# Performance work log

Hardware: AMD Instinct MI355X
Metric: run time of the kernel (lower is better)

## Reference

```python
import jax, jax.numpy as jnp
import numpy as np

V, E, H, S, B, L = 10000, 512, 1024, 64, 64, 2

def setup_inputs() -> dict:
    key = jax.random.key(0)
    ks = iter(jax.random.split(key, 32))
    k_emb = 0.1
    k_h = float(np.sqrt(1.0 / H))
    inp = {}
    inp['inputs'] = jax.random.randint(next(ks), (S, B), 0, V)
    inp['init_hidden'] = jnp.zeros((L, B, H), jnp.float32)
    inp['emb_table'] = jax.random.uniform(next(ks), (V, E), jnp.float32, -k_emb, k_emb)
    in_feats = [E + H, 2 * H]
    for l in range(L):
        fi = in_feats[l]
        for nm in ('Wr', 'Wz', 'Wh'):
            inp[f'{nm}{l}'] = jax.random.uniform(next(ks), (fi, H), jnp.float32, -k_h, k_h)
        for nm in ('br', 'bz', 'bh'):
            inp[f'{nm}{l}'] = jax.random.uniform(next(ks), (H,), jnp.float32, -k_h, k_h)
    inp['Wfc0'] = jax.random.uniform(next(ks), (H, H), jnp.float32, -k_h, k_h)
    inp['bfc0'] = jax.random.uniform(next(ks), (H,), jnp.float32, -k_h, k_h)
    inp['Wout'] = jax.random.uniform(next(ks), (H, V), jnp.float32, -0.1, 0.1)
    inp['bout'] = jnp.zeros((V,), jnp.float32)
    return inp

def reference(inputs, init_hidden, emb_table,
              Wr0, Wz0, Wh0, br0, bz0, bh0,
              Wr1, Wz1, Wh1, br1, bz1, bh1,
              Wfc0, bfc0, Wout, bout):
    layers = [(Wr0, br0, Wz0, bz0, Wh0, bh0), (Wr1, br1, Wz1, bz1, Wh1, bh1)]
    fcs = [(Wfc0, bfc0)]
    emb = emb_table[inputs]  # [S, B, E]

    def step(h_prev, xt):
        # h_prev: [L, B, H]; xt: [B, E]
        x = xt
        hs = []
        for l, (Wr, br, Wz, bz, Wh, bh) in enumerate(layers):
            h = h_prev[l]
            cat = jnp.concatenate([x, h], axis=1)
            r = jax.nn.sigmoid(cat @ Wr + br)
            z = jax.nn.sigmoid(cat @ Wz + bz)
            h_hat = jax.nn.sigmoid(jnp.concatenate([x, r * h], axis=1) @ Wh + bh)
            ht = (1.0 - z) * h + z * h_hat
            hs.append(ht)
            if l < len(layers) - 1:
                Wfc, bfc = fcs[l]
                x = jax.nn.sigmoid(ht @ Wfc + bfc)  # dropout identity (keep_prob=1)
        logits_t = hs[-1] @ Wout + bout  # [B, V]
        return jnp.stack(hs, axis=0), logits_t

    h_final, logits = jax.lax.scan(step, init_hidden, emb)
    return logits, h_final  # [S, B, V], [L, B, H]
```

## Files before the change

kernel.cpp:

```cpp
#include <hip/hip_runtime.h>
#include <hip/hip_bf16.h>

typedef __attribute__((ext_vector_type(8))) short short8;
typedef __attribute__((ext_vector_type(4))) float f32x4;

#define S_ 64
#define B_ 64
#define H_ 1024
#define E_ 512
#define V_ 10000
#define M_ 4096
#define VPAD 10048
#define NBLK 256

__device__ __forceinline__ float sigmoidf_(float x) {
  return 1.0f / (1.0f + __expf(-x));
}

__device__ __forceinline__ void gbar(int* flags, int* gen, int idx) {
  __syncthreads();
  if (blockIdx.x == 0) {
    if (threadIdx.x < 64) {
      int lane = threadIdx.x;
      if (lane == 0)
        __hip_atomic_store(&flags[0], idx, __ATOMIC_RELEASE, __HIP_MEMORY_SCOPE_AGENT);
      for (;;) {
        int v0 = __hip_atomic_load(&flags[lane],       __ATOMIC_RELAXED, __HIP_MEMORY_SCOPE_AGENT);
        int v1 = __hip_atomic_load(&flags[lane + 64],  __ATOMIC_RELAXED, __HIP_MEMORY_SCOPE_AGENT);
        int v2 = __hip_atomic_load(&flags[lane + 128], __ATOMIC_RELAXED, __HIP_MEMORY_SCOPE_AGENT);
        int v3 = __hip_atomic_load(&flags[lane + 192], __ATOMIC_RELAXED, __HIP_MEMORY_SCOPE_AGENT);
        int mn = min(min(v0, v1), min(v2, v3));
        if (__all(mn >= idx)) break;
        __builtin_amdgcn_s_sleep(1);
      }
      __builtin_amdgcn_fence(__ATOMIC_ACQUIRE, "agent");
      if (lane == 0)
        __hip_atomic_store(gen, idx, __ATOMIC_RELEASE, __HIP_MEMORY_SCOPE_AGENT);
    }
  } else {
    if (threadIdx.x == 0) {
      __hip_atomic_store(&flags[blockIdx.x], idx, __ATOMIC_RELEASE, __HIP_MEMORY_SCOPE_AGENT);
      while (__hip_atomic_load(gen, __ATOMIC_RELAXED, __HIP_MEMORY_SCOPE_AGENT) < idx)
        __builtin_amdgcn_s_sleep(1);
      __builtin_amdgcn_fence(__ATOMIC_ACQUIRE, "agent");
    }
  }
  __syncthreads();
}

__global__ void bias_concat(const float* br0, const float* bz0, const float* bh0,
                            const float* br1, const float* bz1, const float* bh1,
                            float* b0cat, float* b1cat) {
  int i = blockIdx.x * 256 + threadIdx.x;
  if (i >= 3072) return;
  if (i < 1024)       { b0cat[i] = br0[i];        b1cat[i] = br1[i]; }
  else if (i < 2048)  { b0cat[i] = bz0[i - 1024]; b1cat[i] = bz1[i - 1024]; }
  else                { b0cat[i] = bh0[i - 2048]; b1cat[i] = bh1[i - 2048]; }
}

__global__ void transpose_cast(const float* __restrict__ src, __hip_bfloat16* __restrict__ dst,
                               int R, int C) {
  __shared__ float tile[32][33];
  int c0 = blockIdx.x * 32, r0 = blockIdx.y * 32;
  int tx = threadIdx.x & 31, ty = threadIdx.x >> 5;
#pragma unroll
  for (int i = 0; i < 4; ++i) {
    int r = r0 + ty + i * 8;
    int c = c0 + tx;
    if (r < R && c < C) tile[ty + i * 8][tx] = src[(size_t)r * C + c];
  }
  __syncthreads();
#pragma unroll
  for (int i = 0; i < 4; ++i) {
    int c = c0 + ty + i * 8;
    int r = r0 + tx;
    if (c < C && r < R) dst[(size_t)c * R + r] = __float2bfloat16(tile[tx][ty + i * 8]);
  }
}

__global__ void embed_cast(const int* __restrict__ inputs, const float* __restrict__ emb,
                           __hip_bfloat16* __restrict__ X0) {
  int idx = blockIdx.x * 256 + threadIdx.x;
  int i = idx >> 7;
  int e4 = idx & 127;
  int tok = inputs[i];
  const float4* src = (const float4*)(emb + (size_t)tok * E_);
  float4 v = src[e4];
  __hip_bfloat16* dst = X0 + (size_t)i * E_ + e4 * 4;
  dst[0] = __float2bfloat16(v.x);
  dst[1] = __float2bfloat16(v.y);
  dst[2] = __float2bfloat16(v.z);
  dst[3] = __float2bfloat16(v.w);
}

__global__ __launch_bounds__(256) void gemm_bf16(
    const __hip_bfloat16* __restrict__ A, const __hip_bfloat16* __restrict__ BT,
    const float* __restrict__ bias, void* __restrict__ C,
    int M, int N, int K, int act, int out_bf16) {
  __shared__ unsigned short Al[64 * 72];
  __shared__ unsigned short Bl[64 * 72];
  const int m0 = blockIdx.y * 64, n0 = blockIdx.x * 64;
  const int tid = threadIdx.x;
  const int wave = tid >> 6, lane = tid & 63;
  const int quad = lane >> 4, lr = lane & 15;
  const int wm = (wave >> 1) * 32, wn = (wave & 1) * 32;
  const int srow = tid >> 2, scol = (tid & 3) << 4;

  f32x4 acc[2][2];
#pragma unroll
  for (int a = 0; a < 2; ++a)
#pragma unroll
    for (int b = 0; b < 2; ++b) acc[a][b] = (f32x4){0.f, 0.f, 0.f, 0.f};

  const __hip_bfloat16* Ag = A + (size_t)(m0 + srow) * K + scol;
  const __hip_bfloat16* Bg = BT + (size_t)(n0 + srow) * K + scol;

  for (int kb = 0; kb < K; kb += 64) {
    short8 a0 = *(const short8*)(Ag + kb);
    short8 a1 = *(const short8*)(Ag + kb + 8);
    short8 b0 = *(const short8*)(Bg + kb);
    short8 b1 = *(const short8*)(Bg + kb + 8);
    *(short8*)&Al[srow * 72 + scol] = a0;
    *(short8*)&Al[srow * 72 + scol + 8] = a1;
    *(short8*)&Bl[srow * 72 + scol] = b0;
    *(short8*)&Bl[srow * 72 + scol + 8] = b1;
    __syncthreads();
#pragma unroll
    for (int k2 = 0; k2 < 64; k2 += 32) {
      short8 af0 = *(const short8*)&Al[(wm + lr) * 72 + k2 + quad * 8];
      short8 af1 = *(const short8*)&Al[(wm + 16 + lr) * 72 + k2 + quad * 8];
      short8 bf0 = *(const short8*)&Bl[(wn + lr) * 72 + k2 + quad * 8];
      short8 bf1 = *(const short8*)&Bl[(wn + 16 + lr) * 72 + k2 + quad * 8];
      acc[0][0] = __builtin_amdgcn_mfma_f32_16x16x32_bf16(af0, bf0, acc[0][0], 0, 0, 0);
      acc[0][1] = __builtin_amdgcn_mfma_f32_16x16x32_bf16(af0, bf1, acc[0][1], 0, 0, 0);
      acc[1][0] = __builtin_amdgcn_mfma_f32_16x16x32_bf16(af1, bf0, acc[1][0], 0, 0, 0);
      acc[1][1] = __builtin_amdgcn_mfma_f32_16x16x32_bf16(af1, bf1, acc[1][1], 0, 0, 0);
    }
    __syncthreads();
  }

#pragma unroll
  for (int mi = 0; mi < 2; ++mi)
#pragma unroll
    for (int ni = 0; ni < 2; ++ni) {
      int n = n0 + wn + ni * 16 + lr;
      if (n >= N) continue;
      float bv = bias ? bias[n] : 0.f;
#pragma unroll
      for (int r = 0; r < 4; ++r) {
        int m = m0 + wm + mi * 16 + quad * 4 + r;
        float v = acc[mi][ni][r] + bv;
        if (act) v = sigmoidf_(v);
        if (out_bf16) ((__hip_bfloat16*)C)[(size_t)m * N + n] = __float2bfloat16(v);
        else          ((float*)C)[(size_t)m * N + n] = v;
      }
    }
}

__global__ __launch_bounds__(256, 1) void gru_fused(
    const float* __restrict__ G0,
    const __hip_bfloat16* __restrict__ W0hT, const __hip_bfloat16* __restrict__ WfcT,
    const __hip_bfloat16* __restrict__ W1xT, const __hip_bfloat16* __restrict__ W1hT,
    const float* __restrict__ bfc, const float* __restrict__ b1cat,
    const float* __restrict__ init_h,
    __hip_bfloat16* __restrict__ h0b, __hip_bfloat16* __restrict__ rh0,
    __hip_bfloat16* __restrict__ h1b, __hip_bfloat16* __restrict__ rh1,
    __hip_bfloat16* __restrict__ x1b, float* __restrict__ g1buf,
    __hip_bfloat16* __restrict__ Hseq1, float* __restrict__ hfin,
    int* __restrict__ bar_flags, int* __restrict__ bar_gen) {
  __shared__ unsigned short Wl[48 * 1032];

  const int bid = blockIdx.x;
  const int gang = bid >> 6;
  const int gid = bid & 63;
  const int tid = threadIdx.x;
  const int wave = tid >> 6, lane = tid & 63;
  const int quad = lane >> 4, lr = lane & 15;

  if (gang == 0 || gang == 3) {
    const __hip_bfloat16* WT = (gang == 0) ? W0hT : W1hT;
    const int nb = gid * 16;
    for (int c = tid; c < 48 * 128; c += 256) {
      int row = c >> 7, col = c & 127;
      int seg = row >> 4, srow = row & 15;
      short8 v = *(const short8*)(WT + (size_t)(seg * 1024 + nb + srow) * H_ + col * 8);
      *(short8*)&Wl[row * 1032 + col * 8] = v;
    }
  } else if (gang == 1) {
    const int nb = gid * 16;
    for (int c = tid; c < 16 * 128; c += 256) {
      int row = c >> 7, col = c & 127;
      short8 v = *(const short8*)(WfcT + (size_t)(nb + row) * H_ + col * 8);
      *(short8*)&Wl[row * 1032 + col * 8] = v;
    }
  } else {
    const int nb = gid * 48;
    for (int c = tid; c < 48 * 128; c += 256) {
      int row = c >> 7, col = c & 127;
      short8 v = *(const short8*)(W1xT + (size_t)(nb + row) * H_ + col * 8);
      *(short8*)&Wl[row * 1032 + col * 8] = v;
    }
  }

  float hreg[4], zreg[4], ghp[4];
  float bias0 = 0.f, bias1 = 0.f, bias2 = 0.f;
  if (gang == 0 || gang == 3) {
    const float* ih = init_h + (gang == 3 ? B_ * H_ : 0);
    __hip_bfloat16* hb = (gang == 0) ? h0b : h1b;
    const int nb = gid * 16;
#pragma unroll
    for (int r = 0; r < 4; ++r) {
      int mm = wave * 16 + quad * 4 + r;
      float v = ih[mm * H_ + nb + lr];
      hreg[r] = v; zreg[r] = 0.f; ghp[r] = 0.f;
      hb[mm * H_ + nb + lr] = __float2bfloat16(v);
    }
  } else if (gang == 1) {
    bias0 = bfc[gid * 16 + lr];
  } else {
    const int nb = gid * 48;
    bias0 = b1cat[nb + lr];
    bias1 = b1cat[nb + 16 + lr];
    bias2 = b1cat[nb + 32 + lr];
  }

  int bidx = 1;
  gbar(bar_flags, bar_gen, bidx++);

  for (int k = 0; k < 132; ++k) {
    if (gang == 0) {
      if (k < 128) {
        const int nb = gid * 16;
        const int am = wave * 16 + lr;
        const int t = k >> 1;
        if (!(k & 1)) {
          float g0v[4], g1v[4];
#pragma unroll
          for (int r = 0; r < 4; ++r) {
            int mm = wave * 16 + quad * 4 + r;
            const float* gp = G0 + (size_t)(t * B_ + mm) * 3072 + nb + lr;
            g0v[r] = gp[0]; g1v[r] = gp[1024]; ghp[r] = gp[2048];
          }
          const __hip_bfloat16* ap = h0b + (size_t)am * H_ + quad * 8;
          short8 areg[32];
#pragma unroll
          for (int kk = 0; kk < 32; ++kk) areg[kk] = *(const short8*)(ap + kk * 32);
          f32x4 acc0 = (f32x4){0.f, 0.f, 0.f, 0.f};
          f32x4 acc1 = (f32x4){0.f, 0.f, 0.f, 0.f};
#pragma unroll
          for (int kk = 0; kk < 32; ++kk) {
            short8 b0 = *(const short8*)&Wl[lr * 1032 + quad * 8 + kk * 32];
            short8 b1 = *(const short8*)&Wl[(16 + lr) * 1032 + quad * 8 + kk * 32];
            acc0 = __builtin_amdgcn_mfma_f32_16x16x32_bf16(areg[kk], b0, acc0, 0, 0, 0);
            acc1 = __builtin_amdgcn_mfma_f32_16x16x32_bf16(areg[kk], b1, acc1, 0, 0, 0);
          }
#pragma unroll
          for (int r = 0; r < 4; ++r) {
            int mm = wave * 16 + quad * 4 + r;
            float rv = sigmoidf_(acc0[r] + g0v[r]);
            zreg[r] = sigmoidf_(acc1[r] + g1v[r]);
            rh0[mm * H_ + nb + lr] = __float2bfloat16(rv * hreg[r]);
          }
        } else {
          const __hip_bfloat16* ap = rh0 + (size_t)am * H_ + quad * 8;
          short8 areg[32];
#pragma unroll
          for (int kk = 0; kk < 32; ++kk) areg[kk] = *(const short8*)(ap + kk * 32);
          f32x4 acc = (f32x4){0.f, 0.f, 0.f, 0.f};
#pragma unroll
          for (int kk = 0; kk < 32; ++kk) {
            short8 b = *(const short8*)&Wl[(32 + lr) * 1032 + quad * 8 + kk * 32];
            acc = __builtin_amdgcn_mfma_f32_16x16x32_bf16(areg[kk], b, acc, 0, 0, 0);
          }
#pragma unroll
          for (int r = 0; r < 4; ++r) {
            int mm = wave * 16 + quad * 4 + r;
            int nn = nb + lr;
            float hh = sigmoidf_(acc[r] + ghp[r]);
            float hn = hreg[r] + zreg[r] * (hh - hreg[r]);
            hreg[r] = hn;
            h0b[mm * H_ + nn] = __float2bfloat16(hn);
            if (t == S_ - 1) hfin[mm * H_ + nn] = hn;
          }
        }
      }
    } else if (gang == 1) {
      if (!(k & 1) && k >= 2 && k <= 128) {
        const int nb = gid * 16;
        const int am = wave * 16 + lr;
        const __hip_bfloat16* ap = h0b + (size_t)am * H_ + quad * 8;
        short8 areg[32];
#pragma unroll
        for (int kk = 0; kk < 32; ++kk) areg[kk] = *(const short8*)(ap + kk * 32);
        f32x4 acc = (f32x4){0.f, 0.f, 0.f, 0.f};
#pragma unroll
        for (int kk = 0; kk < 32; ++kk) {
          short8 b = *(const short8*)&Wl[lr * 1032 + quad * 8 + kk * 32];
          acc = __builtin_amdgcn_mfma_f32_16x16x32_bf16(areg[kk], b, acc, 0, 0, 0);
        }
#pragma unroll
        for (int r = 0; r < 4; ++r) {
          int mm = wave * 16 + quad * 4 + r;
          float v = sigmoidf_(acc[r] + bias0);
          x1b[mm * H_ + nb + lr] = __float2bfloat16(v);
        }
      }
    } else if (gang == 2) {
      if ((k & 1) && k >= 3 && k <= 129) {
        const int nb = gid * 48;
        const int am = wave * 16 + lr;
        const __hip_bfloat16* ap = x1b + (size_t)am * H_ + quad * 8;
        short8 areg[32];
#pragma unroll
        for (int kk = 0; kk < 32; ++kk) areg[kk] = *(const short8*)(ap + kk * 32);
        f32x4 a0 = (f32x4){0.f, 0.f, 0.f, 0.f};
        f32x4 a1 = (f32x4){0.f, 0.f, 0.f, 0.f};
        f32x4 a2 = (f32x4){0.f, 0.f, 0.f, 0.f};
#pragma unroll
        for (int kk = 0; kk < 32; ++kk) {
          short8 b0 = *(const short8*)&Wl[lr * 1032 + quad * 8 + kk * 32];
          short8 b1 = *(const short8*)&Wl[(16 + lr) * 1032 + quad * 8 + kk * 32];
          short8 b2 = *(const short8*)&Wl[(32 + lr) * 1032 + quad * 8 + kk * 32];
          a0 = __builtin_amdgcn_mfma_f32_16x16x32_bf16(areg[kk], b0, a0, 0, 0, 0);
          a1 = __builtin_amdgcn_mfma_f32_16x16x32_bf16(areg[kk], b1, a1, 0, 0, 0);
          a2 = __builtin_amdgcn_mfma_f32_16x16x32_bf16(areg[kk], b2, a2, 0, 0, 0);
        }
#pragma unroll
        for (int r = 0; r < 4; ++r) {
          int mm = wave * 16 + quad * 4 + r;
          float* gp = g1buf + (size_t)mm * 3072 + nb + lr;
          gp[0]  = a0[r] + bias0;
          gp[16] = a1[r] + bias1;
          gp[32] = a2[r] + bias2;
        }
      }
    } else {
      if (k >= 4) {
        const int nb = gid * 16;
        const int am = wave * 16 + lr;
        if (!(k & 1)) {
          if (k <= 130) {
            float g0v[4], g1v[4];
#pragma unroll
            for (int r = 0; r < 4; ++r) {
              int mm = wave * 16 + quad * 4 + r;
              const float* gp = g1buf + (size_t)mm * 3072 + nb + lr;
              g0v[r] = gp[0]; g1v[r] = gp[1024]; ghp[r] = gp[2048];
            }
            const __hip_bfloat16* ap = h1b + (size_t)am * H_ + quad * 8;
            short8 areg[32];
#pragma unroll
            for (int kk = 0; kk < 32; ++kk) areg[kk] = *(const short8*)(ap + kk * 32);
            f32x4 acc0 = (f32x4){0.f, 0.f, 0.f, 0.f};
            f32x4 acc1 = (f32x4){0.f, 0.f, 0.f, 0.f};
#pragma unroll
            for (int kk = 0; kk < 32; ++kk) {
              short8 b0 = *(const short8*)&Wl[lr * 1032 + quad * 8 + kk * 32];
              short8 b1 = *(const short8*)&Wl[(16 + lr) * 1032 + quad * 8 + kk * 32];
              acc0 = __builtin_amdgcn_mfma_f32_16x16x32_bf16(areg[kk], b0, acc0, 0, 0, 0);
              acc1 = __builtin_amdgcn_mfma_f32_16x16x32_bf16(areg[kk], b1, acc1, 0, 0, 0);
            }
#pragma unroll
            for (int r = 0; r < 4; ++r) {
              int mm = wave * 16 + quad * 4 + r;
              float rv = sigmoidf_(acc0[r] + g0v[r]);
              zreg[r] = sigmoidf_(acc1[r] + g1v[r]);
              rh1[mm * H_ + nb + lr] = __float2bfloat16(rv * hreg[r]);
            }
          }
        } else {
          if (k <= 131) {
            const int t = (k - 5) >> 1;
            const __hip_bfloat16* ap = rh1 + (size_t)am * H_ + quad * 8;
            short8 areg[32];
#pragma unroll
            for (int kk = 0; kk < 32; ++kk) areg[kk] = *(const short8*)(ap + kk * 32);
            f32x4 acc = (f32x4){0.f, 0.f, 0.f, 0.f};
#pragma unroll
            for (int kk = 0; kk < 32; ++kk) {
              short8 b = *(const short8*)&Wl[(32 + lr) * 1032 + quad * 8 + kk * 32];
              acc = __builtin_amdgcn_mfma_f32_16x16x32_bf16(areg[kk], b, acc, 0, 0, 0);
            }
#pragma unroll
            for (int r = 0; r < 4; ++r) {
              int mm = wave * 16 + quad * 4 + r;
              int nn = nb + lr;
              float hh = sigmoidf_(acc[r] + ghp[r]);
              float hn = hreg[r] + zreg[r] * (hh - hreg[r]);
              hreg[r] = hn;
              __hip_bfloat16 hb = __float2bfloat16(hn);
              h1b[mm * H_ + nn] = hb;
              Hseq1[(size_t)(t * B_ + mm) * H_ + nn] = hb;
              if (t == S_ - 1) hfin[B_ * H_ + mm * H_ + nn] = hn;
            }
          }
        }
      }
    }
    gbar(bar_flags, bar_gen, bidx++);
  }
}

extern "C" void kernel_launch(void* const* d_in, const int* in_sizes, int n_in,
                              void* d_out, int out_size, void* d_ws, size_t ws_size,
                              hipStream_t stream) {
  const int*   inputs      = (const int*)d_in[0];
  const float* init_hidden = (const float*)d_in[1];
  const float* emb         = (const float*)d_in[2];
  const float* Wr0 = (const float*)d_in[3];
  const float* Wz0 = (const float*)d_in[4];
  const float* Wh0 = (const float*)d_in[5];
  const float* br0 = (const float*)d_in[6];
  const float* bz0 = (const float*)d_in[7];
  const float* bh0 = (const float*)d_in[8];
  const float* Wr1 = (const float*)d_in[9];
  const float* Wz1 = (const float*)d_in[10];
  const float* Wh1 = (const float*)d_in[11];
  const float* br1 = (const float*)d_in[12];
  const float* bz1 = (const float*)d_in[13];
  const float* bh1 = (const float*)d_in[14];
  const float* Wfc0 = (const float*)d_in[15];
  const float* bfc0 = (const float*)d_in[16];
  const float* Wout = (const float*)d_in[17];
  const float* bout = (const float*)d_in[18];
  float* out = (float*)d_out;

  char* ws = (char*)d_ws;
  size_t off = 0;
  auto alloc = [&](size_t bytes) -> char* {
    char* p = ws + off;
    off = (off + bytes + 255) & ~(size_t)255;
    return p;
  };
  int* bar = (int*)alloc(2048);
  __hip_bfloat16* W0xT  = (__hip_bfloat16*)alloc((size_t)3072 * E_ * 2);
  __hip_bfloat16* W0hT  = (__hip_bfloat16*)alloc((size_t)3072 * H_ * 2);
  __hip_bfloat16* WfcT  = (__hip_bfloat16*)alloc((size_t)H_ * H_ * 2);
  __hip_bfloat16* W1xT  = (__hip_bfloat16*)alloc((size_t)3072 * H_ * 2);
  __hip_bfloat16* W1hT  = (__hip_bfloat16*)alloc((size_t)3072 * H_ * 2);
  __hip_bfloat16* WoutT = (__hip_bfloat16*)alloc((size_t)VPAD * H_ * 2);
  float* b0cat = (float*)alloc(3072 * 4);
  float* b1cat = (float*)alloc(3072 * 4);
  __hip_bfloat16* X0    = (__hip_bfloat16*)alloc((size_t)M_ * E_ * 2);
  float* G              = (float*)alloc((size_t)M_ * 3072 * 4);
  __hip_bfloat16* Hseq1 = (__hip_bfloat16*)alloc((size_t)M_ * H_ * 2);
  float* g1buf          = (float*)alloc((size_t)B_ * 3072 * 4);
  __hip_bfloat16* x1b = (__hip_bfloat16*)alloc((size_t)B_ * H_ * 2);
  __hip_bfloat16* hb0 = (__hip_bfloat16*)alloc((size_t)B_ * H_ * 2);
  __hip_bfloat16* hb1 = (__hip_bfloat16*)alloc((size_t)B_ * H_ * 2);
  __hip_bfloat16* rh0 = (__hip_bfloat16*)alloc((size_t)B_ * H_ * 2);
  __hip_bfloat16* rh1 = (__hip_bfloat16*)alloc((size_t)B_ * H_ * 2);
  (void)ws_size; (void)n_in; (void)in_sizes; (void)out_size;

  hipMemsetAsync(bar, 0, 2048, stream);

  hipLaunchKernelGGL(bias_concat, dim3(12), dim3(256), 0, stream,
                     br0, bz0, bh0, br1, bz1, bh1, b0cat, b1cat);

  auto tp = [&](const float* src, __hip_bfloat16* dst, int R, int C) {
    hipLaunchKernelGGL(transpose_cast, dim3((C + 31) / 32, (R + 31) / 32), dim3(256), 0,
                       stream, src, dst, R, C);
  };
  tp(Wr0,            W0xT,                E_, H_);
  tp(Wz0,            W0xT + 1024 * E_,    E_, H_);
  tp(Wh0,            W0xT + 2048 * E_,    E_, H_);
  tp(Wr0 + (size_t)E_ * H_, W0hT,               H_, H_);
  tp(Wz0 + (size_t)E_ * H_, W0hT + 1024 * H_,   H_, H_);
  tp(Wh0 + (size_t)E_ * H_, W0hT + 2048 * H_,   H_, H_);
  tp(Wfc0, WfcT, H_, H_);
  tp(Wr1,            W1xT,                H_, H_);
  tp(Wz1,            W1xT + 1024 * H_,    H_, H_);
  tp(Wh1,            W1xT + 2048 * H_,    H_, H_);
  tp(Wr1 + (size_t)H_ * H_, W1hT,               H_, H_);
  tp(Wz1 + (size_t)H_ * H_, W1hT + 1024 * H_,   H_, H_);
  tp(Wh1 + (size_t)H_ * H_, W1hT + 2048 * H_,   H_, H_);
  tp(Wout, WoutT, H_, V_);

  hipLaunchKernelGGL(embed_cast, dim3(M_ * (E_ / 4) / 256), dim3(256), 0, stream,
                     inputs, emb, X0);

  hipLaunchKernelGGL(gemm_bf16, dim3(3072 / 64, M_ / 64), dim3(256), 0, stream,
                     X0, W0xT, b0cat, (void*)G, M_, 3072, E_, 0, 0);

  {
    const float* Gp = G;
    const __hip_bfloat16* w0h = W0hT; const __hip_bfloat16* wfc = WfcT;
    const __hip_bfloat16* w1x = W1xT; const __hip_bfloat16* w1h = W1hT;
    const float* bfcp = bfc0; const float* b1p = b1cat;
    const float* inith = init_hidden;
    __hip_bfloat16* h0p = hb0; __hip_bfloat16* rh0p = rh0;
    __hip_bfloat16* h1p = hb1; __hip_bfloat16* rh1p = rh1;
    __hip_bfloat16* x1p = x1b; float* g1p = g1buf;
    __hip_bfloat16* Hs1 = Hseq1;
    float* hfin = out + (size_t)M_ * V_;
    int* fl = bar; int* gn = bar + 256;
    void* kargs[] = {(void*)&Gp, (void*)&w0h, (void*)&wfc, (void*)&w1x, (void*)&w1h,
                     (void*)&bfcp, (void*)&b1p, (void*)&inith,
                     (void*)&h0p, (void*)&rh0p, (void*)&h1p, (void*)&rh1p,
                     (void*)&x1p, (void*)&g1p, (void*)&Hs1, (void*)&hfin,
                     (void*)&fl, (void*)&gn};
    hipLaunchCooperativeKernel((const void*)gru_fused, dim3(NBLK), dim3(256),
                               kargs, 0, stream);
  }

  hipLaunchKernelGGL(gemm_bf16, dim3(VPAD / 64, M_ / 64), dim3(256), 0, stream,
                     Hseq1, WoutT, bout, (void*)out, M_, V_, H_, 0, 0);
}
```

Before: 2.525 ms.

## Replace global grid barrier with per-block progress flags and targeted waits

Swaps the centralized all-block barrier in the fused GRU kernel for per-block progress counters. Each gang now waits only on the specific producer gangs it depends on, so stages can run ahead without a full grid rendezvous. h0, x1 and g1 buffers are double-buffered by timestep parity to avoid write-after-read hazards once gangs decouple. The cost is more intricate dependency logic and a greater risk of races if any wait condition is wrong.

```diff
diff --git a/kernel.cpp b/kernel.cpp
--- a/kernel.cpp
+++ b/kernel.cpp
@@ -12,38 +12,32 @@
 #define M_ 4096
 #define VPAD 10048
 #define NBLK 256
+#define BH (B_ * H_)
 
 __device__ __forceinline__ float sigmoidf_(float x) {
   return 1.0f / (1.0f + __expf(-x));
 }
 
-__device__ __forceinline__ void gbar(int* flags, int* gen, int idx) {
+__device__ __forceinline__ void publish(int* prog, int bid, int val, bool rel) {
   __syncthreads();
-  if (blockIdx.x == 0) {
-    if (threadIdx.x < 64) {
-      int lane = threadIdx.x;
-      if (lane == 0)
-        __hip_atomic_store(&flags[0], idx, __ATOMIC_RELEASE, __HIP_MEMORY_SCOPE_AGENT);
-      for (;;) {
-        int v0 = __hip_atomic_load(&flags[lane],       __ATOMIC_RELAXED, __HIP_MEMORY_SCOPE_AGENT);
-        int v1 = __hip_atomic_load(&flags[lane + 64],  __ATOMIC_RELAXED, __HIP_MEMORY_SCOPE_AGENT);
-        int v2 = __hip_atomic_load(&flags[lane + 128], __ATOMIC_RELAXED, __HIP_MEMORY_SCOPE_AGENT);
-        int v3 = __hip_atomic_load(&flags[lane + 192], __ATOMIC_RELAXED, __HIP_MEMORY_SCOPE_AGENT);
-        int mn = min(min(v0, v1), min(v2, v3));
-        if (__all(mn >= idx)) break;
-        __builtin_amdgcn_s_sleep(1);
-      }
-      __builtin_amdgcn_fence(__ATOMIC_ACQUIRE, "agent");
-      if (lane == 0)
-        __hip_atomic_store(gen, idx, __ATOMIC_RELEASE, __HIP_MEMORY_SCOPE_AGENT);
-    }
-  } else {
-    if (threadIdx.x == 0) {
-      __hip_atomic_store(&flags[blockIdx.x], idx, __ATOMIC_RELEASE, __HIP_MEMORY_SCOPE_AGENT);
-      while (__hip_atomic_load(gen, __ATOMIC_RELAXED, __HIP_MEMORY_SCOPE_AGENT) < idx)
-        __builtin_amdgcn_s_sleep(1);
-      __builtin_amdgcn_fence(__ATOMIC_ACQUIRE, "agent");
-    }
+  if (threadIdx.x == 0) {
+    if (rel) __hip_atomic_store(&prog[bid], val, __ATOMIC_RELEASE, __HIP_MEMORY_SCOPE_AGENT);
+    else     __hip_atomic_store(&prog[bid], val, __ATOMIC_RELAXED, __HIP_MEMORY_SCOPE_AGENT);
+  }
+}
+__device__ __forceinline__ void wait_two(int* prog, int b0, int r0, int b1, int r1) {
+  if (threadIdx.x < 64) {
+    int l = threadIdx.x;
+    for (;;) {
+      bool ok = __hip_atomic_load(&prog[b0 + l], __ATOMIC_RELAXED,
+                                  __HIP_MEMORY_SCOPE_AGENT) >= r0;
+      if (b1 >= 0)
+        ok &= __hip_atomic_load(&prog[b1 + l], __ATOMIC_RELAXED,
+                                __HIP_MEMORY_SCOPE_AGENT) >= r1;
+      if (__all(ok)) break;
+      __builtin_amdgcn_s_sleep(1);
+    }
+    __builtin_amdgcn_fence(__ATOMIC_ACQUIRE, "agent");
   }
   __syncthreads();
 }
@@ -167,7 +161,7 @@
     __hip_bfloat16* __restrict__ h1b, __hip_bfloat16* __restrict__ rh1,
     __hip_bfloat16* __restrict__ x1b, float* __restrict__ g1buf,
     __hip_bfloat16* __restrict__ Hseq1, float* __restrict__ hfin,
-    int* __restrict__ bar_flags, int* __restrict__ bar_gen) {
+    int* __restrict__ prog) {
   __shared__ unsigned short Wl[48 * 1032];
 
   const int bid = blockIdx.x;
@@ -205,8 +199,8 @@
   float hreg[4], zreg[4], ghp[4];
   float bias0 = 0.f, bias1 = 0.f, bias2 = 0.f;
   if (gang == 0 || gang == 3) {
-    const float* ih = init_h + (gang == 3 ? B_ * H_ : 0);
-    __hip_bfloat16* hb = (gang == 0) ? h0b : h1b;
+    const float* ih = init_h + (gang == 3 ? BH : 0);
+    __hip_bfloat16* hb = (gang == 0) ? (h0b + BH) : h1b;
     const int nb = gid * 16;
 #pragma unroll
     for (int r = 0; r < 4; ++r) {
@@ -223,17 +217,18 @@
     bias1 = b1cat[nb + 16 + lr];
     bias2 = b1cat[nb + 32 + lr];
   }
-
-  int bidx = 1;
-  gbar(bar_flags, bar_gen, bidx++);
+  publish(prog, bid, 1, gang == 0 || gang == 3);
 
   for (int k = 0; k < 132; ++k) {
+    bool active = false;
     if (gang == 0) {
       if (k < 128) {
+        active = true;
         const int nb = gid * 16;
         const int am = wave * 16 + lr;
         const int t = k >> 1;
         if (!(k & 1)) {
+          wait_two(prog, 0, k + 1, -1, 0);
           float g0v[4], g1v[4];
 #pragma unroll
           for (int r = 0; r < 4; ++r) {
@@ -241,7 +236,7 @@
             const float* gp = G0 + (size_t)(t * B_ + mm) * 3072 + nb + lr;
             g0v[r] = gp[0]; g1v[r] = gp[1024]; ghp[r] = gp[2048];
           }
-          const __hip_bfloat16* ap = h0b + (size_t)am * H_ + quad * 8;
+          const __hip_bfloat16* ap = h0b + (size_t)((t + 1) & 1) * BH + (size_t)am * H_ + quad * 8;
           short8 areg[32];
 #pragma unroll
           for (int kk = 0; kk < 32; ++kk) areg[kk] = *(const short8*)(ap + kk * 32);
@@ -262,6 +257,7 @@
             rh0[mm * H_ + nb + lr] = __float2bfloat16(rv * hreg[r]);
           }
         } else {
+          wait_two(prog, 0, k + 1, 64, k - 1);
           const __hip_bfloat16* ap = rh0 + (size_t)am * H_ + quad * 8;
           short8 areg[32];
 #pragma unroll
@@ -272,6 +268,7 @@
             short8 b = *(const short8*)&Wl[(32 + lr) * 1032 + quad * 8 + kk * 32];
             acc = __builtin_amdgcn_mfma_f32_16x16x32_bf16(areg[kk], b, acc, 0, 0, 0);
           }
+          __hip_bfloat16* hw = h0b + (size_t)(t & 1) * BH;
 #pragma unroll
           for (int r = 0; r < 4; ++r) {
             int mm = wave * 16 + quad * 4 + r;
@@ -279,16 +276,19 @@
             float hh = sigmoidf_(acc[r] + ghp[r]);
             float hn = hreg[r] + zreg[r] * (hh - hreg[r]);
             hreg[r] = hn;
-            h0b[mm * H_ + nn] = __float2bfloat16(hn);
+            hw[mm * H_ + nn] = __float2bfloat16(hn);
             if (t == S_ - 1) hfin[mm * H_ + nn] = hn;
           }
         }
       }
     } else if (gang == 1) {
       if (!(k & 1) && k >= 2 && k <= 128) {
+        active = true;
+        wait_two(prog, 0, k + 1, 128, k - 1);
+        const int t = (k - 2) >> 1;
         const int nb = gid * 16;
         const int am = wave * 16 + lr;
-        const __hip_bfloat16* ap = h0b + (size_t)am * H_ + quad * 8;
+        const __hip_bfloat16* ap = h0b + (size_t)(t & 1) * BH + (size_t)am * H_ + quad * 8;
         short8 areg[32];
 #pragma unroll
         for (int kk = 0; kk < 32; ++kk) areg[kk] = *(const short8*)(ap + kk * 32);
@@ -298,18 +298,22 @@
           short8 b = *(const short8*)&Wl[lr * 1032 + quad * 8 + kk * 32];
           acc = __builtin_amdgcn_mfma_f32_16x16x32_bf16(areg[kk], b, acc, 0, 0, 0);
         }
+        __hip_bfloat16* xw = x1b + (size_t)(t & 1) * BH;
 #pragma unroll
         for (int r = 0; r < 4; ++r) {
           int mm = wave * 16 + quad * 4 + r;
           float v = sigmoidf_(acc[r] + bias0);
-          x1b[mm * H_ + nb + lr] = __float2bfloat16(v);
+          xw[mm * H_ + nb + lr] = __float2bfloat16(v);
         }
       }
     } else if (gang == 2) {
       if ((k & 1) && k >= 3 && k <= 129) {
+        active = true;
+        wait_two(prog, 64, k + 1, 192, k - 1);
+        const int t = (k - 3) >> 1;
         const int nb = gid * 48;
         const int am = wave * 16 + lr;
-        const __hip_bfloat16* ap = x1b + (size_t)am * H_ + quad * 8;
+        const __hip_bfloat16* ap = x1b + (size_t)(t & 1) * BH + (size_t)am * H_ + quad * 8;
         short8 areg[32];
 #pragma unroll
         for (int kk = 0; kk < 32; ++kk) areg[kk] = *(const short8*)(ap + kk * 32);
@@ -325,79 +329,84 @@
           a1 = __builtin_amdgcn_mfma_f32_16x16x32_bf16(areg[kk], b1, a1, 0, 0, 0);
           a2 = __builtin_amdgcn_mfma_f32_16x16x32_bf16(areg[kk], b2, a2, 0, 0, 0);
         }
+        float* gw = g1buf + (size_t)(t & 1) * (B_ * 3072);
 #pragma unroll
         for (int r = 0; r < 4; ++r) {
           int mm = wave * 16 + quad * 4 + r;
-          float* gp = g1buf + (size_t)mm * 3072 + nb + lr;
+          float* gp = gw + (size_t)mm * 3072 + nb + lr;
           gp[0]  = a0[r] + bias0;
           gp[16] = a1[r] + bias1;
           gp[32] = a2[r] + bias2;
         }
       }
     } else {
-      if (k >= 4) {
-        const int nb = gid * 16;
-        const int am = wave * 16 + lr;
-        if (!(k & 1)) {
-          if (k <= 130) {
-            float g0v[4], g1v[4];
-#pragma unroll
-            for (int r = 0; r < 4; ++r) {
-              int mm = wave * 16 + quad * 4 + r;
-              const float* gp = g1buf + (size_t)mm * 3072 + nb + lr;
-              g0v[r] = gp[0]; g1v[r] = gp[1024]; ghp[r] = gp[2048];
-            }
-            const __hip_bfloat16* ap = h1b + (size_t)am * H_ + quad * 8;
-            short8 areg[32];
-#pragma unroll
-            for (int kk = 0; kk < 32; ++kk) areg[kk] = *(const short8*)(ap + kk * 32);
-            f32x4 acc0 = (f32x4){0.f, 0.f, 0.f, 0.f};
-            f32x4 acc1 = (f32x4){0.f, 0.f, 0.f, 0.f};
-#pragma unroll
-            for (int kk = 0; kk < 32; ++kk) {
-              short8 b0 = *(const short8*)&Wl[lr * 1032 + quad * 8 + kk * 32];
-              short8 b1 = *(const short8*)&Wl[(16 + lr) * 1032 + quad * 8 + kk * 32];
-              acc0 = __builtin_amdgcn_mfma_f32_16x16x32_bf16(areg[kk], b0, acc0, 0, 0, 0);
-              acc1 = __builtin_amdgcn_mfma_f32_16x16x32_bf16(areg[kk], b1, acc1, 0, 0, 0);
-            }
-#pragma unroll
-            for (int r = 0; r < 4; ++r) {
-              int mm = wave * 16 + quad * 4 + r;
-              float rv = sigmoidf_(acc0[r] + g0v[r]);
-              zreg[r] = sigmoidf_(acc1[r] + g1v[r]);
-              rh1[mm * H_ + nb + lr] = __float2bfloat16(rv * hreg[r]);
-            }
-          }
-        } else {
-          if (k <= 131) {
-            const int t = (k - 5) >> 1;
-            const __hip_bfloat16* ap = rh1 + (size_t)am * H_ + quad * 8;
-            short8 areg[32];
-#pragma unroll
-            for (int kk = 0; kk < 32; ++kk) areg[kk] = *(const short8*)(ap + kk * 32);
-            f32x4 acc = (f32x4){0.f, 0.f, 0.f, 0.f};
-#pragma unroll
-            for (int kk = 0; kk < 32; ++kk) {
-              short8 b = *(const short8*)&Wl[(32 + lr) * 1032 + quad * 8 + kk * 32];
-              acc = __builtin_amdgcn_mfma_f32_16x16x32_bf16(areg[kk], b, acc, 0, 0, 0);
-            }
-#pragma unroll
-            for (int r = 0; r < 4; ++r) {
-              int mm = wave * 16 + quad * 4 + r;
-              int nn = nb + lr;
-              float hh = sigmoidf_(acc[r] + ghp[r]);
-              float hn = hreg[r] + zreg[r] * (hh - hreg[r]);
-              hreg[r] = hn;
-              __hip_bfloat16 hb = __float2bfloat16(hn);
-              h1b[mm * H_ + nn] = hb;
-              Hseq1[(size_t)(t * B_ + mm) * H_ + nn] = hb;
-              if (t == S_ - 1) hfin[B_ * H_ + mm * H_ + nn] = hn;
-            }
+      const int nb = gid * 16;
+      const int am = wave * 16 + lr;
+      if (!(k & 1)) {
+        if (k >= 4 && k <= 130) {
+          active = true;
+          wait_two(prog, 128, k + 1, 192, k + 1);
+          const int t = (k - 4) >> 1;
+          const float* gr = g1buf + (size_t)(t & 1) * (B_ * 3072);
+          float g0v[4], g1v[4];
+#pragma unroll
+          for (int r = 0; r < 4; ++r) {
+            int mm = wave * 16 + quad * 4 + r;
+            const float* gp = gr + (size_t)mm * 3072 + nb + lr;
+            g0v[r] = gp[0]; g1v[r] = gp[1024]; ghp[r] = gp[2048];
+          }
+          const __hip_bfloat16* ap = h1b + (size_t)am * H_ + quad * 8;
+          short8 areg[32];
+#pragma unroll
+          for (int kk = 0; kk < 32; ++kk) areg[kk] = *(const short8*)(ap + kk * 32);
+          f32x4 acc0 = (f32x4){0.f, 0.f, 0.f, 0.f};
+          f32x4 acc1 = (f32x4){0.f, 0.f, 0.f, 0.f};
+#pragma unroll
+          for (int kk = 0; kk < 32; ++kk) {
+            short8 b0 = *(const short8*)&Wl[lr * 1032 + quad * 8 + kk * 32];
+            short8 b1 = *(const short8*)&Wl[(16 + lr) * 1032 + quad * 8 + kk * 32];
+            acc0 = __builtin_amdgcn_mfma_f32_16x16x32_bf16(areg[kk], b0, acc0, 0, 0, 0);
+            acc1 = __builtin_amdgcn_mfma_f32_16x16x32_bf16(areg[kk], b1, acc1, 0, 0, 0);
+          }
+#pragma unroll
+          for (int r = 0; r < 4; ++r) {
+            int mm = wave * 16 + quad * 4 + r;
+            float rv = sigmoidf_(acc0[r] + g0v[r]);
+            zreg[r] = sigmoidf_(acc1[r] + g1v[r]);
+            rh1[mm * H_ + nb + lr] = __float2bfloat16(rv * hreg[r]);
+          }
+        }
+      } else {
+        if (k >= 5 && k <= 131) {
+          active = true;
+          wait_two(prog, 192, k + 1, -1, 0);
+          const int t = (k - 5) >> 1;
+          const __hip_bfloat16* ap = rh1 + (size_t)am * H_ + quad * 8;
+          short8 areg[32];
+#pragma unroll
+          for (int kk = 0; kk < 32; ++kk) areg[kk] = *(const short8*)(ap + kk * 32);
+          f32x4 acc = (f32x4){0.f, 0.f, 0.f, 0.f};
+#pragma unroll
+          for (int kk = 0; kk < 32; ++kk) {
+            short8 b = *(const short8*)&Wl[(32 + lr) * 1032 + quad * 8 + kk * 32];
+            acc = __builtin_amdgcn_mfma_f32_16x16x32_bf16(areg[kk], b, acc, 0, 0, 0);
+          }
+#pragma unroll
+          for (int r = 0; r < 4; ++r) {
+            int mm = wave * 16 + quad * 4 + r;
+            int nn = nb + lr;
+            float hh = sigmoidf_(acc[r] + ghp[r]);
+            float hn = hreg[r] + zreg[r] * (hh - hreg[r]);
+            hreg[r] = hn;
+            __hip_bfloat16 hb = __float2bfloat16(hn);
+            h1b[mm * H_ + nn] = hb;
+            Hseq1[(size_t)(t * B_ + mm) * H_ + nn] = hb;
+            if (t == S_ - 1) hfin[BH + mm * H_ + nn] = hn;
           }
         }
       }
     }
-    gbar(bar_flags, bar_gen, bidx++);
+    publish(prog, bid, k + 2, active);
   }
 }
 
@@ -432,7 +441,7 @@
     off = (off + bytes + 255) & ~(size_t)255;
     return p;
   };
-  int* bar = (int*)alloc(2048);
+  int* prog = (int*)alloc(2048);
   __hip_bfloat16* W0xT  = (__hip_bfloat16*)alloc((size_t)3072 * E_ * 2);
   __hip_bfloat16* W0hT  = (__hip_bfloat16*)alloc((size_t)3072 * H_ * 2);
   __hip_bfloat16* WfcT  = (__hip_bfloat16*)alloc((size_t)H_ * H_ * 2);
@@ -444,15 +453,15 @@
   __hip_bfloat16* X0    = (__hip_bfloat16*)alloc((size_t)M_ * E_ * 2);
   float* G              = (float*)alloc((size_t)M_ * 3072 * 4);
   __hip_bfloat16* Hseq1 = (__hip_bfloat16*)alloc((size_t)M_ * H_ * 2);
-  float* g1buf          = (float*)alloc((size_t)B_ * 3072 * 4);
-  __hip_bfloat16* x1b = (__hip_bfloat16*)alloc((size_t)B_ * H_ * 2);
-  __hip_bfloat16* hb0 = (__hip_bfloat16*)alloc((size_t)B_ * H_ * 2);
-  __hip_bfloat16* hb1 = (__hip_bfloat16*)alloc((size_t)B_ * H_ * 2);
-  __hip_bfloat16* rh0 = (__hip_bfloat16*)alloc((size_t)B_ * H_ * 2);
-  __hip_bfloat16* rh1 = (__hip_bfloat16*)alloc((size_t)B_ * H_ * 2);
+  float* g1buf          = (float*)alloc((size_t)2 * B_ * 3072 * 4);
+  __hip_bfloat16* h0b = (__hip_bfloat16*)alloc((size_t)2 * BH * 2);
+  __hip_bfloat16* x1b = (__hip_bfloat16*)alloc((size_t)2 * BH * 2);
+  __hip_bfloat16* h1b = (__hip_bfloat16*)alloc((size_t)BH * 2);
+  __hip_bfloat16* rh0 = (__hip_bfloat16*)alloc((size_t)BH * 2);
+  __hip_bfloat16* rh1 = (__hip_bfloat16*)alloc((size_t)BH * 2);
   (void)ws_size; (void)n_in; (void)in_sizes; (void)out_size;
 
-  hipMemsetAsync(bar, 0, 2048, stream);
+  hipMemsetAsync(prog, 0, 2048, stream);
 
   hipLaunchKernelGGL(bias_concat, dim3(12), dim3(256), 0, stream,
                      br0, bz0, bh0, br1, bz1, bh1, b0cat, b1cat);
@@ -488,17 +497,17 @@
     const __hip_bfloat16* w1x = W1xT; const __hip_bfloat16* w1h = W1hT;
     const float* bfcp = bfc0; const float* b1p = b1cat;
     const float* inith = init_hidden;
-    __hip_bfloat16* h0p = hb0; __hip_bfloat16* rh0p = rh0;
-    __hip_bfloat16* h1p = hb1; __hip_bfloat16* rh1p = rh1;
+    __hip_bfloat16* h0p = h0b; __hip_bfloat16* rh0p = rh0;
+    __hip_bfloat16* h1p = h1b; __hip_bfloat16* rh1p = rh1;
     __hip_bfloat16* x1p = x1b; float* g1p = g1buf;
     __hip_bfloat16* Hs1 = Hseq1;
     float* hfin = out + (size_t)M_ * V_;
-    int* fl = bar; int* gn = bar + 256;
+    int* pg = prog;
     void* kargs[] = {(void*)&Gp, (void*)&w0h, (void*)&wfc, (void*)&w1x, (void*)&w1h,
                      (void*)&bfcp, (void*)&b1p, (void*)&inith,
                      (void*)&h0p, (void*)&rh0p, (void*)&h1p, (void*)&rh1p,
                      (void*)&x1p, (void*)&g1p, (void*)&Hs1, (void*)&hfin,
-                     (void*)&fl, (void*)&gn};
+                     (void*)&pg};
     hipLaunchCooperativeKernel((const void*)gru_fused, dim3(NBLK), dim3(256),
                                kargs, 0, stream);
   }
```

Result: faster. 2.393 ms (-5.2%).
